# Kernel tuning notes

Hardware: AMD Instinct MI355X
Metric: run time of the kernel (lower is better)

The kernel has to match this reference:

```python
import jax, jax.numpy as jnp
import numpy as np

S = 128  # sqrt_n; feature dim n = S*S = 16384


def _perm(x, s):
    # rearrange '... (m n) -> ... (n m)' with m = n = s: transpose the s x s
    # factorization of the last dim.
    return jnp.swapaxes(x.reshape(*x.shape[:-1], s, s), -1, -2).reshape(x.shape)


def _bdmm(x, w):
    # blockdiag_matmul: view last dim as (blocks=s, m=s), per-block GEMM.
    b, m = w.shape[0], w.shape[-1]
    xv = x.reshape(*x.shape[:-1], b, m)
    return jnp.einsum('bnm,...bm->...bn', w, xv).reshape(x.shape)


def setup_inputs() -> dict:
    key = jax.random.key(0)
    k1, k2, k3, k4 = jax.random.split(key, 4)
    n = S * S
    scale = jnp.float32(1.0 / np.sqrt(S))
    return {
        'x': jax.random.normal(k1, (2, 2048, n), dtype=jnp.float32),
        'L': jax.random.normal(k2, (S, S, S), dtype=jnp.float32) * scale,
        'R': jax.random.normal(k3, (S, S, S), dtype=jnp.float32) * scale,
        'bias': jax.random.normal(k4, (n,), dtype=jnp.float32) * jnp.float32(0.02),
    }


def reference(x, L, R, bias):
    s = L.shape[0]
    x = _perm(x, s)
    x = _bdmm(x, L)
    x = _perm(x, s)
    x = _bdmm(x, R)
    x = _perm(x, s)
    return x + bias
```

## Files before the change

### kernel.cpp

```cpp
#include <hip/hip_runtime.h>

typedef __bf16 bf16x8 __attribute__((ext_vector_type(8)));
typedef float  f32x4  __attribute__((ext_vector_type(4)));

static __device__ __forceinline__ unsigned short f32_to_bf16(float f) {
  union { float f; unsigned u; } v; v.f = f;
  unsigned r = v.u + 0x7fffu + ((v.u >> 16) & 1u);
  return (unsigned short)(r >> 16);
}

__global__ __launch_bounds__(256) void k_cvt2(const float* __restrict__ L,
                                              const float* __restrict__ R,
                                              unsigned short* __restrict__ Lb,
                                              unsigned short* __restrict__ Rb) {
  int i = blockIdx.x * 256 + threadIdx.x;
  const float* s; unsigned short* d; int idx;
  if (i < 524288) { s = L; d = Lb; idx = i; } else { s = R; d = Rb; idx = i - 524288; }
  float4 v = ((const float4*)s)[idx];
  uint2 o;
  o.x = (unsigned)f32_to_bf16(v.x) | ((unsigned)f32_to_bf16(v.y) << 16);
  o.y = (unsigned)f32_to_bf16(v.z) | ((unsigned)f32_to_bf16(v.w) << 16);
  ((uint2*)d)[idx] = o;
}

__global__ __launch_bounds__(256, 1) void k_stageA(const float* __restrict__ x,
                                                   const unsigned short* __restrict__ Lb,
                                                   unsigned short* __restrict__ T) {
  __shared__ unsigned short Xs[65536];
  const int bid = blockIdx.x;
  const int m0 = (bid & 7) << 4;
  const int r0 = (bid >> 3) << 5;
  const int tid = threadIdx.x;
  const int w = tid >> 6, lane = tid & 63;

  {
    const int mg = lane & 3, kg = lane >> 2;
#pragma unroll
    for (int it = 0; it < 8; ++it) {
      const int r = (it << 2) + w;
      const float* g = x + (size_t)(r0 + r) * 16384 + m0 + (mg << 2);
      float4 v[8];
#pragma unroll
      for (int kk = 0; kk < 8; ++kk) v[kk] = *(const float4*)(g + (((kg << 3) + kk) << 7));
      const int cw = (kg ^ (r & 15)) << 3;
#pragma unroll
      for (int mm = 0; mm < 4; ++mm) {
        unsigned short o[8];
#pragma unroll
        for (int kk = 0; kk < 8; ++kk) o[kk] = f32_to_bf16(((const float*)&v[kk])[mm]);
        *(uint4*)&Xs[((((mg << 2) + mm) << 5) + r) * 128 + cw] = *(const uint4*)o;
      }
    }
  }
  __syncthreads();

  const int l16 = lane & 15, q = lane >> 4;
  const int mloc = w << 2;
#pragma unroll
  for (int jt = 0; jt < 8; ++jt) {
    const int j0 = jt << 4;
    f32x4 acc[4][2] = {};
#pragma unroll
    for (int ks = 0; ks < 4; ++ks) {
#pragma unroll
      for (int mi = 0; mi < 4; ++mi) {
        const bf16x8 bfrag = *(const bf16x8*)(Lb + (size_t)(m0 + mloc + mi) * 16384
                                              + ((j0 + l16) << 7) + (ks << 5) + (q << 3));
#pragma unroll
        for (int rf = 0; rf < 2; ++rf) {
          const int row = ((mloc + mi) << 5) + (rf << 4) + l16;
          const bf16x8 afrag = *(const bf16x8*)&Xs[row * 128 + ((((ks << 2) + q) ^ l16) << 3)];
          acc[mi][rf] = __builtin_amdgcn_mfma_f32_16x16x32_bf16(afrag, bfrag, acc[mi][rf], 0, 0, 0);
        }
      }
    }
#pragma unroll
    for (int mi = 0; mi < 4; ++mi) {
      unsigned short* tp = T + (size_t)(m0 + mloc + mi) * 524288
                             + ((size_t)(j0 + l16) << 12) + r0 + (q << 2);
#pragma unroll
      for (int rf = 0; rf < 2; ++rf) {
        unsigned short o[4];
#pragma unroll
        for (int p = 0; p < 4; ++p) o[p] = f32_to_bf16(acc[mi][rf][p]);
        *(uint2*)(tp + (rf << 4)) = *(const uint2*)o;
      }
    }
  }
}

__global__ __launch_bounds__(256, 1) void k_stageB(const unsigned short* __restrict__ T,
                                                   const unsigned short* __restrict__ Rb,
                                                   const float* __restrict__ bias,
                                                   float* __restrict__ out) {
  __shared__ unsigned short Ts[65536];
  const int bid = blockIdx.x;
  const int j0 = (bid & 7) << 4;
  const int r0 = (bid >> 3) << 5;
  const int tid = threadIdx.x;

  {
#pragma unroll
    for (int it = 0; it < 4; ++it) {
      const int flat = (it << 8) + tid;
      const int rc = flat & 3, jj = (flat >> 2) & 15, mc = flat >> 6;
      uint4 v[8];
#pragma unroll
      for (int mm = 0; mm < 8; ++mm)
        v[mm] = *(const uint4*)(T + (size_t)((mc << 3) + mm) * 524288
                                + ((size_t)(j0 + jj) << 12) + r0 + (rc << 3));
      const unsigned short* s = (const unsigned short*)v;
#pragma unroll
      for (int rr = 0; rr < 8; ++rr) {
        unsigned short o[8];
#pragma unroll
        for (int mm = 0; mm < 8; ++mm) o[mm] = s[(mm << 3) + rr];
        const int row = (jj << 5) + (rc << 3) + rr;
        *(uint4*)&Ts[row * 128 + ((mc ^ (row & 15)) << 3)] = *(const uint4*)o;
      }
    }
  }
  __syncthreads();

  const int w = tid >> 6, lane = tid & 63, l16 = lane & 15, q = lane >> 4;
#pragma unroll
  for (int ph = 0; ph < 2; ++ph) {
    const int ib = (ph << 6) + (w << 4);
    f32x4 acc[16][2] = {};
#pragma unroll
    for (int ms = 0; ms < 4; ++ms) {
#pragma unroll
      for (int jb = 0; jb < 16; ++jb) {
        const bf16x8 af = *(const bf16x8*)(Rb + (size_t)(j0 + jb) * 16384
                                           + ((ib + l16) << 7) + (ms << 5) + (q << 3));
#pragma unroll
        for (int rf = 0; rf < 2; ++rf) {
          const int row = (jb << 5) + (rf << 4) + l16;
          const bf16x8 bf = *(const bf16x8*)&Ts[row * 128 + ((((ms << 2) + q) ^ l16) << 3)];
          acc[jb][rf] = __builtin_amdgcn_mfma_f32_16x16x32_bf16(af, bf, acc[jb][rf], 0, 0, 0);
        }
      }
    }
#pragma unroll
    for (int p = 0; p < 4; ++p) {
      const int i = ib + (q << 2) + p;
      const float* bp = bias + (i << 7) + j0;
      const float4 b0 = *(const float4*)(bp + 0), b1 = *(const float4*)(bp + 4),
                   b2 = *(const float4*)(bp + 8), b3 = *(const float4*)(bp + 12);
#pragma unroll
      for (int rf = 0; rf < 2; ++rf) {
        float* op = out + ((size_t)(r0 + (rf << 4) + l16) << 14) + (i << 7) + j0;
        float4 o0, o1, o2, o3;
        o0.x = acc[0][rf][p] + b0.x;  o0.y = acc[1][rf][p] + b0.y;
        o0.z = acc[2][rf][p] + b0.z;  o0.w = acc[3][rf][p] + b0.w;
        o1.x = acc[4][rf][p] + b1.x;  o1.y = acc[5][rf][p] + b1.y;
        o1.z = acc[6][rf][p] + b1.z;  o1.w = acc[7][rf][p] + b1.w;
        o2.x = acc[8][rf][p] + b2.x;  o2.y = acc[9][rf][p] + b2.y;
        o2.z = acc[10][rf][p] + b2.z; o2.w = acc[11][rf][p] + b2.w;
        o3.x = acc[12][rf][p] + b3.x; o3.y = acc[13][rf][p] + b3.y;
        o3.z = acc[14][rf][p] + b3.z; o3.w = acc[15][rf][p] + b3.w;
        *(float4*)(op + 0)  = o0; *(float4*)(op + 4)  = o1;
        *(float4*)(op + 8)  = o2; *(float4*)(op + 12) = o3;
      }
    }
  }
}

extern "C" void kernel_launch(void* const* d_in, const int* in_sizes, int n_in,
                              void* d_out, int out_size, void* d_ws, size_t ws_size,
                              hipStream_t stream) {
  const float* x    = (const float*)d_in[0];
  const float* L    = (const float*)d_in[1];
  const float* R    = (const float*)d_in[2];
  const float* bias = (const float*)d_in[3];
  float* out = (float*)d_out;

  const size_t SZ_W = (size_t)4 << 20;
  const size_t SZ_T = (size_t)128 << 20;
  if (ws_size < 2 * SZ_W + SZ_T) return;

  char* ws = (char*)d_ws;
  unsigned short* Lb = (unsigned short*)ws;
  unsigned short* Rb = (unsigned short*)(ws + SZ_W);
  unsigned short* Tw = (unsigned short*)(ws + 2 * SZ_W);

  k_cvt2<<<4096, 256, 0, stream>>>(L, R, Lb, Rb);
  k_stageA<<<1024, 256, 0, stream>>>(x, Lb, Tw);
  k_stageB<<<1024, 256, 0, stream>>>(Tw, Rb, bias, out);
}
```

Before: 770.4 us.

## Shrink stage tiles, chunk K through smaller LDS, and change intermediate layout

```diff
diff --git a/kernel.cpp b/kernel.cpp
--- a/kernel.cpp
+++ b/kernel.cpp
@@ -7,6 +7,10 @@
   union { float f; unsigned u; } v; v.f = f;
   unsigned r = v.u + 0x7fffu + ((v.u >> 16) & 1u);
   return (unsigned short)(r >> 16);
+}
+
+static __device__ __forceinline__ int swz(int row) {
+  return (row ^ (row >> 4) ^ (row >> 7)) & 7;
 }
 
 __global__ __launch_bounds__(256) void k_cvt2(const float* __restrict__ L,
@@ -23,145 +27,127 @@
   ((uint2*)d)[idx] = o;
 }
 
-__global__ __launch_bounds__(256, 1) void k_stageA(const float* __restrict__ x,
+__global__ __launch_bounds__(256, 4) void k_stageA(const float* __restrict__ x,
                                                    const unsigned short* __restrict__ Lb,
                                                    unsigned short* __restrict__ T) {
-  __shared__ unsigned short Xs[65536];
+  __shared__ unsigned short Xs[16 * 16 * 64];
   const int bid = blockIdx.x;
-  const int m0 = (bid & 7) << 4;
-  const int r0 = (bid >> 3) << 5;
+  const int u = bid & 7, jh = (bid >> 3) & 1, mh = (bid >> 4) & 1;
+  const int rest = bid >> 5;
+  const int mc = rest & 3, rtt = rest >> 2;
+  const int r0 = (rtt * 8 + u) << 4;
+  const int m0 = ((mc << 1) + mh) << 4;
   const int tid = threadIdx.x;
   const int w = tid >> 6, lane = tid & 63;
+  const int l16 = lane & 15, q = lane >> 4;
+  const int j0w = ((jh << 2) + w) << 4;
 
-  {
-    const int mg = lane & 3, kg = lane >> 2;
+  const int mg = tid & 3, rq = (tid >> 2) & 3, kg = tid >> 4;
+  f32x4 acc[16] = {};
+  const unsigned short* Lbase = Lb + (size_t)m0 * 16384 + ((j0w + l16) << 7) + (q << 3);
+
 #pragma unroll
-    for (int it = 0; it < 8; ++it) {
-      const int r = (it << 2) + w;
-      const float* g = x + (size_t)(r0 + r) * 16384 + m0 + (mg << 2);
-      float4 v[8];
+  for (int kr = 0; kr < 2; ++kr) {
+    if (kr) __syncthreads();
 #pragma unroll
-      for (int kk = 0; kk < 8; ++kk) v[kk] = *(const float4*)(g + (((kg << 3) + kk) << 7));
-      const int cw = (kg ^ (r & 15)) << 3;
+    for (int rr = 0; rr < 4; ++rr) {
+      const int r = (rr << 2) + rq;
+      const float* g = x + (size_t)(r0 + r) * 16384 + ((kr << 6) + (kg << 2)) * 128 + m0 + (mg << 2);
+      float4 v0 = *(const float4*)(g);
+      float4 v1 = *(const float4*)(g + 128);
+      float4 v2 = *(const float4*)(g + 256);
+      float4 v3 = *(const float4*)(g + 384);
 #pragma unroll
       for (int mm = 0; mm < 4; ++mm) {
-        unsigned short o[8];
+        const int row = (((mg << 2) + mm) << 4) + r;
+        unsigned short o[4] = { f32_to_bf16(((const float*)&v0)[mm]),
+                                f32_to_bf16(((const float*)&v1)[mm]),
+                                f32_to_bf16(((const float*)&v2)[mm]),
+                                f32_to_bf16(((const float*)&v3)[mm]) };
+        *(uint2*)((char*)Xs + row * 128 + (((kg >> 1) ^ swz(row)) << 4) + ((kg & 1) << 3)) =
+            *(const uint2*)o;
+      }
+    }
+    __syncthreads();
 #pragma unroll
-        for (int kk = 0; kk < 8; ++kk) o[kk] = f32_to_bf16(((const float*)&v[kk])[mm]);
-        *(uint4*)&Xs[((((mg << 2) + mm) << 5) + r) * 128 + cw] = *(const uint4*)o;
+    for (int ksl = 0; ksl < 2; ++ksl) {
+#pragma unroll
+      for (int mb = 0; mb < 16; ++mb) {
+        const bf16x8 af = *(const bf16x8*)(Lbase + (size_t)mb * 16384 + (kr << 6) + (ksl << 5));
+        const int row = (mb << 4) + l16;
+        const bf16x8 bf = *(const bf16x8*)((const char*)Xs + row * 128
+                                           + ((((ksl << 2) + q) ^ swz(row)) << 4));
+        acc[mb] = __builtin_amdgcn_mfma_f32_16x16x32_bf16(af, bf, acc[mb], 0, 0, 0);
       }
     }
   }
-  __syncthreads();
+#pragma unroll
+  for (int p = 0; p < 4; ++p) {
+    const int j = j0w + (q << 2) + p;
+    unsigned short o[16];
+#pragma unroll
+    for (int mb = 0; mb < 16; ++mb) o[mb] = f32_to_bf16(acc[mb][p]);
+    unsigned short* tp = T + (size_t)j * 524288 + ((size_t)(r0 + l16) << 7) + m0;
+    *(uint4*)tp = *(const uint4*)o;
+    *(uint4*)(tp + 8) = *(const uint4*)(o + 8);
+  }
+}
 
+__global__ __launch_bounds__(512, 4) void k_stageB(const unsigned short* __restrict__ T,
+                                                   const unsigned short* __restrict__ Rb,
+                                                   const float* __restrict__ bias,
+                                                   float* __restrict__ out) {
+  __shared__ unsigned short Ts[16 * 16 * 64];
+  const int bid = blockIdx.x;
+  const int j0 = (bid & 7) << 4;
+  const int r0 = (bid >> 3) << 4;
+  const int tid = threadIdx.x;
+  const int w = tid >> 6, lane = tid & 63;
   const int l16 = lane & 15, q = lane >> 4;
-  const int mloc = w << 2;
+  const int ib = w << 4;
+
+  f32x4 acc[16] = {};
+  const unsigned short* Rbase = Rb + (size_t)j0 * 16384 + ((ib + l16) << 7) + (q << 3);
+
 #pragma unroll
-  for (int jt = 0; jt < 8; ++jt) {
-    const int j0 = jt << 4;
-    f32x4 acc[4][2] = {};
+  for (int mr = 0; mr < 2; ++mr) {
+    if (mr) __syncthreads();
 #pragma unroll
-    for (int ks = 0; ks < 4; ++ks) {
+    for (int it = 0; it < 4; ++it) {
+      const int flat = (it << 9) + tid;
+      const int c8 = flat & 7, r = (flat >> 3) & 15, jj = flat >> 7;
+      const uint4 v = *(const uint4*)(T + (size_t)(j0 + jj) * 524288
+                                      + ((size_t)(r0 + r) << 7) + (mr << 6) + (c8 << 3));
+      const int row = (jj << 4) + r;
+      *(uint4*)((char*)Ts + row * 128 + ((c8 ^ swz(row)) << 4)) = v;
+    }
+    __syncthreads();
 #pragma unroll
-      for (int mi = 0; mi < 4; ++mi) {
-        const bf16x8 bfrag = *(const bf16x8*)(Lb + (size_t)(m0 + mloc + mi) * 16384
-                                              + ((j0 + l16) << 7) + (ks << 5) + (q << 3));
+    for (int msl = 0; msl < 2; ++msl) {
 #pragma unroll
-        for (int rf = 0; rf < 2; ++rf) {
-          const int row = ((mloc + mi) << 5) + (rf << 4) + l16;
-          const bf16x8 afrag = *(const bf16x8*)&Xs[row * 128 + ((((ks << 2) + q) ^ l16) << 3)];
-          acc[mi][rf] = __builtin_amdgcn_mfma_f32_16x16x32_bf16(afrag, bfrag, acc[mi][rf], 0, 0, 0);
-        }
-      }
-    }
-#pragma unroll
-    for (int mi = 0; mi < 4; ++mi) {
-      unsigned short* tp = T + (size_t)(m0 + mloc + mi) * 524288
-                             + ((size_t)(j0 + l16) << 12) + r0 + (q << 2);
-#pragma unroll
-      for (int rf = 0; rf < 2; ++rf) {
-        unsigned short o[4];
-#pragma unroll
-        for (int p = 0; p < 4; ++p) o[p] = f32_to_bf16(acc[mi][rf][p]);
-        *(uint2*)(tp + (rf << 4)) = *(const uint2*)o;
+      for (int jb = 0; jb < 16; ++jb) {
+        const bf16x8 af = *(const bf16x8*)(Rbase + (size_t)jb * 16384 + (mr << 6) + (msl << 5));
+        const int row = (jb << 4) + l16;
+        const bf16x8 bf = *(const bf16x8*)((const char*)Ts + row * 128
+                                           + ((((msl << 2) + q) ^ swz(row)) << 4));
+        acc[jb] = __builtin_amdgcn_mfma_f32_16x16x32_bf16(af, bf, acc[jb], 0, 0, 0);
       }
     }
   }
-}
-
-__global__ __launch_bounds__(256, 1) void k_stageB(const unsigned short* __restrict__ T,
-                                                   const unsigned short* __restrict__ Rb,
-                                                   const float* __restrict__ bias,
-                                                   float* __restrict__ out) {
-  __shared__ unsigned short Ts[65536];
-  const int bid = blockIdx.x;
-  const int j0 = (bid & 7) << 4;
-  const int r0 = (bid >> 3) << 5;
-  const int tid = threadIdx.x;
-
-  {
 #pragma unroll
-    for (int it = 0; it < 4; ++it) {
-      const int flat = (it << 8) + tid;
-      const int rc = flat & 3, jj = (flat >> 2) & 15, mc = flat >> 6;
-      uint4 v[8];
+  for (int p = 0; p < 4; ++p) {
+    const int i = ib + (q << 2) + p;
+    const float* bp = bias + (i << 7) + j0;
+    float* op = out + ((size_t)(r0 + l16) << 14) + (i << 7) + j0;
 #pragma unroll
-      for (int mm = 0; mm < 8; ++mm)
-        v[mm] = *(const uint4*)(T + (size_t)((mc << 3) + mm) * 524288
-                                + ((size_t)(j0 + jj) << 12) + r0 + (rc << 3));
-      const unsigned short* s = (const unsigned short*)v;
-#pragma unroll
-      for (int rr = 0; rr < 8; ++rr) {
-        unsigned short o[8];
-#pragma unroll
-        for (int mm = 0; mm < 8; ++mm) o[mm] = s[(mm << 3) + rr];
-        const int row = (jj << 5) + (rc << 3) + rr;
-        *(uint4*)&Ts[row * 128 + ((mc ^ (row & 15)) << 3)] = *(const uint4*)o;
-      }
-    }
-  }
-  __syncthreads();
-
-  const int w = tid >> 6, lane = tid & 63, l16 = lane & 15, q = lane >> 4;
-#pragma unroll
-  for (int ph = 0; ph < 2; ++ph) {
-    const int ib = (ph << 6) + (w << 4);
-    f32x4 acc[16][2] = {};
-#pragma unroll
-    for (int ms = 0; ms < 4; ++ms) {
-#pragma unroll
-      for (int jb = 0; jb < 16; ++jb) {
-        const bf16x8 af = *(const bf16x8*)(Rb + (size_t)(j0 + jb) * 16384
-                                           + ((ib + l16) << 7) + (ms << 5) + (q << 3));
-#pragma unroll
-        for (int rf = 0; rf < 2; ++rf) {
-          const int row = (jb << 5) + (rf << 4) + l16;
-          const bf16x8 bf = *(const bf16x8*)&Ts[row * 128 + ((((ms << 2) + q) ^ l16) << 3)];
-          acc[jb][rf] = __builtin_amdgcn_mfma_f32_16x16x32_bf16(af, bf, acc[jb][rf], 0, 0, 0);
-        }
-      }
-    }
-#pragma unroll
-    for (int p = 0; p < 4; ++p) {
-      const int i = ib + (q << 2) + p;
-      const float* bp = bias + (i << 7) + j0;
-      const float4 b0 = *(const float4*)(bp + 0), b1 = *(const float4*)(bp + 4),
-                   b2 = *(const float4*)(bp + 8), b3 = *(const float4*)(bp + 12);
-#pragma unroll
-      for (int rf = 0; rf < 2; ++rf) {
-        float* op = out + ((size_t)(r0 + (rf << 4) + l16) << 14) + (i << 7) + j0;
-        float4 o0, o1, o2, o3;
-        o0.x = acc[0][rf][p] + b0.x;  o0.y = acc[1][rf][p] + b0.y;
-        o0.z = acc[2][rf][p] + b0.z;  o0.w = acc[3][rf][p] + b0.w;
-        o1.x = acc[4][rf][p] + b1.x;  o1.y = acc[5][rf][p] + b1.y;
-        o1.z = acc[6][rf][p] + b1.z;  o1.w = acc[7][rf][p] + b1.w;
-        o2.x = acc[8][rf][p] + b2.x;  o2.y = acc[9][rf][p] + b2.y;
-        o2.z = acc[10][rf][p] + b2.z; o2.w = acc[11][rf][p] + b2.w;
-        o3.x = acc[12][rf][p] + b3.x; o3.y = acc[13][rf][p] + b3.y;
-        o3.z = acc[14][rf][p] + b3.z; o3.w = acc[15][rf][p] + b3.w;
-        *(float4*)(op + 0)  = o0; *(float4*)(op + 4)  = o1;
-        *(float4*)(op + 8)  = o2; *(float4*)(op + 12) = o3;
-      }
+    for (int g4 = 0; g4 < 4; ++g4) {
+      float4 b = *(const float4*)(bp + (g4 << 2));
+      float4 o;
+      o.x = acc[(g4 << 2) + 0][p] + b.x;
+      o.y = acc[(g4 << 2) + 1][p] + b.y;
+      o.z = acc[(g4 << 2) + 2][p] + b.z;
+      o.w = acc[(g4 << 2) + 3][p] + b.w;
+      *(float4*)(op + (g4 << 2)) = o;
     }
   }
 }
@@ -185,6 +171,6 @@
   unsigned short* Tw = (unsigned short*)(ws + 2 * SZ_W);
 
   k_cvt2<<<4096, 256, 0, stream>>>(L, R, Lb, Rb);
-  k_stageA<<<1024, 256, 0, stream>>>(x, Lb, Tw);
-  k_stageB<<<1024, 256, 0, stream>>>(Tw, Rb, bias, out);
+  k_stageA<<<4096, 256, 0, stream>>>(x, Lb, Tw);
+  k_stageB<<<2048, 512, 0, stream>>>(Tw, Rb, bias, out);
 }
```

After: 828.7 us. 7.6% more time.
